# Optimization experiments

Hardware: AMD Instinct MI355X
Metric: run time of the kernel (lower is better)

The kernel has to match this reference:

```python
import jax, jax.numpy as jnp
import numpy as np

B, L, H, DK, DV, D, FC, NL = 8, 2016, 4, 32, 32, 256, 64, 3
EPS = 1e-5
SCALE = 1.0 / np.sqrt(float(D))  # module uses 1/sqrt(d_model), not 1/sqrt(dim_k)


def _ln(x, g, b):
    m = jnp.mean(x, axis=-1, keepdims=True)
    v = jnp.mean((x - m) ** 2, axis=-1, keepdims=True)
    return (x - m) * jax.lax.rsqrt(v + EPS) * g + b


def setup_inputs() -> dict:
    key = jax.random.key(0)
    ks = iter(jax.random.split(key, 32))

    def lin(k, shape, fan_in):
        # torch nn.Linear default: U(-1/sqrt(fan_in), 1/sqrt(fan_in))
        lim = 1.0 / np.sqrt(float(fan_in))
        return jax.random.uniform(k, shape, minval=-lim, maxval=lim, dtype=jnp.float32)

    inp = {
        'x': jax.random.normal(next(ks), (B, L, 2), dtype=jnp.float32),
        'in_w': lin(next(ks), (2, D), 2),
        'in_b': lin(next(ks), (D,), 2),
        'qw': lin(next(ks), (NL, D, H * DK), D),
        'qb': lin(next(ks), (NL, H * DK), D),
        'kw': lin(next(ks), (NL, D, H * DK), D),
        'kb': lin(next(ks), (NL, H * DK), D),
        'vw': lin(next(ks), (NL, D, H * DV), D),
        'vb': lin(next(ks), (NL, H * DV), D),
        'ow': lin(next(ks), (NL, H * DV, D), H * DV),
        'ob': lin(next(ks), (NL, D), H * DV),
        'f1w': lin(next(ks), (NL, D, FC), D),
        'f1b': lin(next(ks), (NL, FC), D),
        'f2w': lin(next(ks), (NL, FC, D), FC),
        'f2b': lin(next(ks), (NL, D), FC),
        'n1g': jnp.ones((NL, D), jnp.float32),
        'n1b': jnp.zeros((NL, D), jnp.float32),
        'n2g': jnp.ones((NL, D), jnp.float32),
        'n2b': jnp.zeros((NL, D), jnp.float32),
        'o1w': lin(next(ks), (D, D), D),
        'o1b': lin(next(ks), (D,), D),
        'o2w': lin(next(ks), (D, 2), D),
        'o2b': lin(next(ks), (2,), D),
    }
    return inp


def reference(x, in_w, in_b, qw, qb, kw, kb, vw, vb, ow, ob,
              f1w, f1b, f2w, f2b, n1g, n1b, n2g, n2b,
              o1w, o1b, o2w, o2b):
    h = x @ in_w + in_b  # (B, L, D)
    attns = []
    for i in range(NL):
        Q = (h @ qw[i] + qb[i]).reshape(B, L, H, DK)
        K = (h @ kw[i] + kb[i]).reshape(B, L, H, DK)
        V = (h @ vw[i] + vb[i]).reshape(B, L, H, DV)
        scores = jnp.einsum('blhe,bshe->bhls', Q, K) * SCALE  # (B,H,L,L)
        scores = jax.nn.softmax(scores, axis=-1)
        o = jnp.einsum('bhls,bshd->blhd', scores, V).reshape(B, L, H * DV)
        h = _ln(h + (o @ ow[i] + ob[i]), n1g[i], n1b[i])  # dropout is identity at eval
        ff = jax.nn.relu(h @ f1w[i] + f1b[i]) @ f2w[i] + f2b[i]
        h = _ln(h + ff, n2g[i], n2b[i])
        attns.append(scores)
    out = jax.nn.relu(h @ o1w + o1b) @ o2w + o2b  # (B, L, 2)
    return (out, jnp.stack(attns))
```

## Files before the change

### kernel.cpp

```cpp
#include <hip/hip_runtime.h>

typedef __attribute__((ext_vector_type(8))) short bh8;
typedef __attribute__((ext_vector_type(4))) float f32x4;

#define NB   8
#define NLAY 3
#define LSEQ 2016
#define NH   4
#define DM   256
#define FCN  64
#define MR   (NB*LSEQ)
#define SCL  0.0625f
#define SP   2024

__device__ __forceinline__ float b2f(unsigned short u) {
  union { unsigned int i; float f; } c; c.i = ((unsigned int)u) << 16; return c.f;
}
__device__ __forceinline__ unsigned short f2b(float f) {
  union { float f; unsigned int i; } c; c.f = f;
  unsigned int r = c.i + 0x7fffu + ((c.i >> 16) & 1u);
  return (unsigned short)(r >> 16);
}

__global__ __launch_bounds__(256) void k_f2bf(const float* __restrict__ s,
    unsigned short* __restrict__ d, int n) {
  int i = blockIdx.x * 256 + threadIdx.x;
  if (i < n) d[i] = f2b(s[i]);
}

__global__ __launch_bounds__(256) void k_embed(const float* __restrict__ x,
    const float* __restrict__ w, const float* __restrict__ bias,
    float* __restrict__ h, unsigned short* __restrict__ hb) {
  int m = blockIdx.x, d = threadIdx.x;
  float v = x[m*2] * w[d] + x[m*2+1] * w[DM + d] + bias[d];
  size_t idx = (size_t)m * DM + d;
  h[idx] = v;
  hb[idx] = f2b(v);
}

template<int MODE, int RELU>
__global__ __launch_bounds__(256) void k_gemm(
    const unsigned short* __restrict__ A, const unsigned short* __restrict__ W,
    const float* __restrict__ bias, const float* __restrict__ res,
    void* __restrict__ outp, int M, int N, int K)
{
  __shared__ unsigned short As[64 * 40];
  __shared__ unsigned short Ws[64 * 40];
  const int t = threadIdx.x;
  const int lane = t & 63, w = t >> 6;
  const int bm = blockIdx.y << 6, bn = blockIdx.x << 6;
  const int mw = (w & 1) << 5, nw = (w >> 1) << 5;
  const int q = lane >> 4, r = lane & 15;
  const int am = t >> 2, akc = (t & 3) << 3;
  const int wk = t >> 3, wnc = (t & 7) << 3;

  f32x4 zero = {0.f, 0.f, 0.f, 0.f};
  f32x4 acc[2][2] = {{zero, zero}, {zero, zero}};

  for (int k0 = 0; k0 < K; k0 += 32) {
    uint4 av = *(const uint4*)(A + (size_t)(bm + am) * K + k0 + akc);
    *(uint4*)(As + am * 40 + akc) = av;
    union { uint4 u; unsigned short s[8]; } wv;
    wv.u = *(const uint4*)(W + (size_t)(k0 + wk) * N + bn + wnc);
    #pragma unroll
    for (int j = 0; j < 8; ++j) Ws[(wnc + j) * 40 + wk] = wv.s[j];
    __syncthreads();

    bh8 a0 = *(const bh8*)(As + (mw + r) * 40 + (q << 3));
    bh8 a1 = *(const bh8*)(As + (mw + 16 + r) * 40 + (q << 3));
    bh8 b0 = *(const bh8*)(Ws + (nw + r) * 40 + (q << 3));
    bh8 b1 = *(const bh8*)(Ws + (nw + 16 + r) * 40 + (q << 3));
    acc[0][0] = __builtin_amdgcn_mfma_f32_16x16x32_bf16(a0, b0, acc[0][0], 0, 0, 0);
    acc[0][1] = __builtin_amdgcn_mfma_f32_16x16x32_bf16(a0, b1, acc[0][1], 0, 0, 0);
    acc[1][0] = __builtin_amdgcn_mfma_f32_16x16x32_bf16(a1, b0, acc[1][0], 0, 0, 0);
    acc[1][1] = __builtin_amdgcn_mfma_f32_16x16x32_bf16(a1, b1, acc[1][1], 0, 0, 0);
    __syncthreads();
  }

  #pragma unroll
  for (int mi = 0; mi < 2; ++mi)
  #pragma unroll
  for (int ni = 0; ni < 2; ++ni)
  #pragma unroll
  for (int rr = 0; rr < 4; ++rr) {
    int gm = bm + mw + (mi << 4) + (q << 2) + rr;
    int gn = bn + nw + (ni << 4) + r;
    float v = acc[mi][ni][rr] + bias[gn];
    if (RELU) v = v > 0.f ? v : 0.f;
    if (MODE == 0) {
      ((unsigned short*)outp)[(size_t)gm * N + gn] = f2b(v);
    } else if (MODE == 1) {
      int b = gm / LSEQ, l = gm - b * LSEQ;
      int hh = gn >> 5, e = gn & 31;
      ((unsigned short*)outp)[((((size_t)b * NH + hh) * LSEQ + l) << 5) + e] = f2b(v);
    } else if (MODE == 2) {
      int b = gm / LSEQ, l = gm - b * LSEQ;
      int hh = gn >> 5, e = gn & 31;
      ((unsigned short*)outp)[(((size_t)b * NH + hh) * 32 + e) * LSEQ + l] = f2b(v);
    } else {
      size_t idx = (size_t)gm * DM + gn;
      ((float*)outp)[idx] = v + res[idx];
    }
  }
}

__global__ __launch_bounds__(256) void k_ln(const float* __restrict__ y,
    const float* __restrict__ g, const float* __restrict__ bta,
    float* __restrict__ h, unsigned short* __restrict__ hb)
{
  int t = threadIdx.x, lane = t & 63, w = t >> 6;
  int row = blockIdx.x * 4 + w;
  const float* yr = y + (size_t)row * DM;
  float4 v = *(const float4*)(yr + lane * 4);
  float s = v.x + v.y + v.z + v.w;
  float sq = v.x * v.x + v.y * v.y + v.z * v.z + v.w * v.w;
  #pragma unroll
  for (int m = 1; m < 64; m <<= 1) { s += __shfl_xor(s, m, 64); sq += __shfl_xor(sq, m, 64); }
  float mean = s * (1.f / 256.f);
  float var = sq * (1.f / 256.f) - mean * mean;
  float rs = rsqrtf(var + 1e-5f);
  float4 gg = *(const float4*)(g + lane * 4);
  float4 bb = *(const float4*)(bta + lane * 4);
  float4 o;
  o.x = (v.x - mean) * rs * gg.x + bb.x;
  o.y = (v.y - mean) * rs * gg.y + bb.y;
  o.z = (v.z - mean) * rs * gg.z + bb.z;
  o.w = (v.w - mean) * rs * gg.w + bb.w;
  *(float4*)(h + (size_t)row * DM + lane * 4) = o;
  ushort4 u;
  u.x = f2b(o.x); u.y = f2b(o.y); u.z = f2b(o.z); u.w = f2b(o.w);
  *(ushort4*)(hb + (size_t)row * DM + lane * 4) = u;
}

__global__ __launch_bounds__(256) void k_attn(
    const unsigned short* __restrict__ Qb, const unsigned short* __restrict__ Kb,
    const unsigned short* __restrict__ Vt, float* __restrict__ Pout,
    unsigned short* __restrict__ ao)
{
  __shared__ unsigned short S[16 * SP];
  __shared__ float red[4 * 16 * 32];
  __shared__ float rinv[16];
  const int t = threadIdx.x, lane = t & 63, w = t >> 6;
  const int bid = blockIdx.x;
  const int rb = bid % 126, bh = bid / 126;
  const int l0 = rb << 4;
  const int q = lane >> 4, r = lane & 15;

  bh8 qf = *(const bh8*)(Qb + (((size_t)bh * LSEQ + l0 + r) << 5) + (q << 3));
  for (int st = w; st < 126; st += 4) {
    int s0 = st << 4;
    bh8 kf = *(const bh8*)(Kb + (((size_t)bh * LSEQ + s0 + r) << 5) + (q << 3));
    f32x4 c = {0.f, 0.f, 0.f, 0.f};
    c = __builtin_amdgcn_mfma_f32_16x16x32_bf16(qf, kf, c, 0, 0, 0);
    #pragma unroll
    for (int rr = 0; rr < 4; ++rr)
      S[(q * 4 + rr) * SP + s0 + r] = f2b(c[rr] * SCL);
  }
  __syncthreads();

  {
    int row = t >> 4, c = t & 15;
    float mx = -1e30f;
    for (int col = c; col < LSEQ; col += 16)
      mx = fmaxf(mx, b2f(S[row * SP + col]));
    #pragma unroll
    for (int m = 1; m < 16; m <<= 1) mx = fmaxf(mx, __shfl_xor(mx, m, 64));
    float sum = 0.f;
    for (int col = c; col < LSEQ; col += 16) {
      float e = __expf(b2f(S[row * SP + col]) - mx);
      sum += e;
      S[row * SP + col] = f2b(e);
    }
    #pragma unroll
    for (int m = 1; m < 16; m <<= 1) sum += __shfl_xor(sum, m, 64);
    if (c == 0) rinv[row] = 1.f / sum;
  }
  __syncthreads();

  float* prow0 = Pout + (size_t)bh * LSEQ * LSEQ + (size_t)l0 * LSEQ;
  for (int row = 0; row < 16; ++row) {
    float iv = rinv[row];
    float* pr = prow0 + (size_t)row * LSEQ;
    for (int col = t; col < LSEQ; col += 256)
      pr[col] = b2f(S[row * SP + col]) * iv;
  }

  f32x4 o0 = {0.f, 0.f, 0.f, 0.f}, o1 = {0.f, 0.f, 0.f, 0.f};
  const unsigned short* vtb = Vt + (size_t)bh * 32 * LSEQ;
  for (int st = w; st < 63; st += 4) {
    int s0 = st << 5;
    bh8 pf = *(const bh8*)(S + r * SP + s0 + (q << 3));
    bh8 v0 = *(const bh8*)(vtb + (size_t)r * LSEQ + s0 + (q << 3));
    bh8 v1 = *(const bh8*)(vtb + (size_t)(16 + r) * LSEQ + s0 + (q << 3));
    o0 = __builtin_amdgcn_mfma_f32_16x16x32_bf16(pf, v0, o0, 0, 0, 0);
    o1 = __builtin_amdgcn_mfma_f32_16x16x32_bf16(pf, v1, o1, 0, 0, 0);
  }
  float* rw = red + w * 512;
  #pragma unroll
  for (int rr = 0; rr < 4; ++rr) {
    rw[(q * 4 + rr) * 32 + r] = o0[rr];
    rw[(q * 4 + rr) * 32 + 16 + r] = o1[rr];
  }
  __syncthreads();
  for (int idx = t; idx < 512; idx += 256) {
    int row = idx >> 5, d = idx & 31;
    float v = red[idx] + red[512 + idx] + red[1024 + idx] + red[1536 + idx];
    v *= rinv[row];
    int b = bh >> 2, hh = bh & 3;
    ao[(size_t)(b * LSEQ + l0 + row) * 128 + (hh << 5) + d] = f2b(v);
  }
}

__global__ __launch_bounds__(256) void k_head(const unsigned short* __restrict__ t1,
    const float* __restrict__ o2w, const float* __restrict__ o2b,
    float* __restrict__ outp)
{
  int t = threadIdx.x, lane = t & 63, w = t >> 6;
  int row = blockIdx.x * 4 + w;
  union { ushort4 u; unsigned short s[4]; } pk;
  pk.u = *(const ushort4*)(t1 + (size_t)row * DM + lane * 4);
  float a0 = 0.f, a1 = 0.f;
  #pragma unroll
  for (int j = 0; j < 4; ++j) {
    float xv = b2f(pk.s[j]);
    int k = lane * 4 + j;
    a0 += xv * o2w[k * 2];
    a1 += xv * o2w[k * 2 + 1];
  }
  #pragma unroll
  for (int m = 1; m < 64; m <<= 1) { a0 += __shfl_xor(a0, m, 64); a1 += __shfl_xor(a1, m, 64); }
  if (lane == 0) {
    outp[(size_t)row * 2]     = a0 + o2b[0];
    outp[(size_t)row * 2 + 1] = a1 + o2b[1];
  }
}

extern "C" void kernel_launch(void* const* d_in, const int* in_sizes, int n_in,
                              void* d_out, int out_size, void* d_ws, size_t ws_size,
                              hipStream_t stream) {
  const float* x    = (const float*)d_in[0];
  const float* in_w = (const float*)d_in[1];
  const float* in_b = (const float*)d_in[2];
  const float* qw   = (const float*)d_in[3];
  const float* qb   = (const float*)d_in[4];
  const float* kw   = (const float*)d_in[5];
  const float* kb   = (const float*)d_in[6];
  const float* vw   = (const float*)d_in[7];
  const float* vb   = (const float*)d_in[8];
  const float* ow   = (const float*)d_in[9];
  const float* ob   = (const float*)d_in[10];
  const float* f1w  = (const float*)d_in[11];
  const float* f1b  = (const float*)d_in[12];
  const float* f2w  = (const float*)d_in[13];
  const float* f2b  = (const float*)d_in[14];
  const float* n1g  = (const float*)d_in[15];
  const float* n1b  = (const float*)d_in[16];
  const float* n2g  = (const float*)d_in[17];
  const float* n2b  = (const float*)d_in[18];
  const float* o1w  = (const float*)d_in[19];
  const float* o1b  = (const float*)d_in[20];
  const float* o2w  = (const float*)d_in[21];
  const float* o2b  = (const float*)d_in[22];

  char* p = (char*)d_ws;
  auto alloc = [&](size_t bytes) { char* r = p; p += (bytes + 255) & ~(size_t)255; return r; };
  float*          h    = (float*)alloc((size_t)MR * DM * 4);
  unsigned short* hb   = (unsigned short*)alloc((size_t)MR * DM * 2);
  float*          tmp  = (float*)alloc((size_t)MR * DM * 4);
  unsigned short* Qb   = (unsigned short*)alloc((size_t)MR * 128 * 2);
  unsigned short* Kb   = (unsigned short*)alloc((size_t)MR * 128 * 2);
  unsigned short* Vt   = (unsigned short*)alloc((size_t)MR * 128 * 2);
  unsigned short* ao   = (unsigned short*)alloc((size_t)MR * 128 * 2);
  unsigned short* Fb   = (unsigned short*)alloc((size_t)MR * FCN * 2);
  unsigned short* t1   = (unsigned short*)alloc((size_t)MR * DM * 2);
  unsigned short* qwb  = (unsigned short*)alloc(98304 * 2);
  unsigned short* kwb  = (unsigned short*)alloc(98304 * 2);
  unsigned short* vwb  = (unsigned short*)alloc(98304 * 2);
  unsigned short* owb  = (unsigned short*)alloc(98304 * 2);
  unsigned short* f1wb = (unsigned short*)alloc(49152 * 2);
  unsigned short* f2wb = (unsigned short*)alloc(49152 * 2);
  unsigned short* o1wb = (unsigned short*)alloc(65536 * 2);

  k_f2bf<<<(98304 + 255) / 256, 256, 0, stream>>>(qw, qwb, 98304);
  k_f2bf<<<(98304 + 255) / 256, 256, 0, stream>>>(kw, kwb, 98304);
  k_f2bf<<<(98304 + 255) / 256, 256, 0, stream>>>(vw, vwb, 98304);
  k_f2bf<<<(98304 + 255) / 256, 256, 0, stream>>>(ow, owb, 98304);
  k_f2bf<<<(49152 + 255) / 256, 256, 0, stream>>>(f1w, f1wb, 49152);
  k_f2bf<<<(49152 + 255) / 256, 256, 0, stream>>>(f2w, f2wb, 49152);
  k_f2bf<<<(65536 + 255) / 256, 256, 0, stream>>>(o1w, o1wb, 65536);

  k_embed<<<MR, 256, 0, stream>>>(x, in_w, in_b, h, hb);

  float* outp = (float*)d_out;
  for (int i = 0; i < NLAY; ++i) {
    k_gemm<1, 0><<<dim3(2, 252), 256, 0, stream>>>(hb, qwb + i * 32768, qb + i * 128, nullptr, Qb, MR, 128, 256);
    k_gemm<1, 0><<<dim3(2, 252), 256, 0, stream>>>(hb, kwb + i * 32768, kb + i * 128, nullptr, Kb, MR, 128, 256);
    k_gemm<2, 0><<<dim3(2, 252), 256, 0, stream>>>(hb, vwb + i * 32768, vb + i * 128, nullptr, Vt, MR, 128, 256);
    k_attn<<<4032, 256, 0, stream>>>(Qb, Kb, Vt,
        outp + 32256 + (size_t)i * NB * NH * LSEQ * LSEQ, ao);
    k_gemm<3, 0><<<dim3(4, 252), 256, 0, stream>>>(ao, owb + i * 32768, ob + i * 256, h, tmp, MR, 256, 128);
    k_ln<<<MR / 4, 256, 0, stream>>>(tmp, n1g + i * 256, n1b + i * 256, h, hb);
    k_gemm<0, 1><<<dim3(1, 252), 256, 0, stream>>>(hb, f1wb + i * 16384, f1b + i * 64, nullptr, Fb, MR, 64, 256);
    k_gemm<3, 0><<<dim3(4, 252), 256, 0, stream>>>(Fb, f2wb + i * 16384, f2b + i * 256, h, tmp, MR, 256, 64);
    k_ln<<<MR / 4, 256, 0, stream>>>(tmp, n2g + i * 256, n2b + i * 256, h, hb);
  }
  k_gemm<0, 1><<<dim3(4, 252), 256, 0, stream>>>(hb, o1wb, o1b, nullptr, t1, MR, 256, 256);
  k_head<<<MR / 4, 256, 0, stream>>>(t1, o2w, o2b, outp);
}
```

Measured before the change: 2.572 ms.

## Rewrite attention as two-pass online softmax with per-wave tiles and prefetch GEMM loads

```diff
diff --git a/kernel.cpp b/kernel.cpp
--- a/kernel.cpp
+++ b/kernel.cpp
@@ -11,7 +11,7 @@
 #define FCN  64
 #define MR   (NB*LSEQ)
 #define SCL  0.0625f
-#define SP   2024
+#define TP   40
 
 __device__ __forceinline__ float b2f(unsigned short u) {
   union { unsigned int i; float f; } c; c.i = ((unsigned int)u) << 16; return c.f;
@@ -20,6 +20,11 @@
   union { float f; unsigned int i; } c; c.f = f;
   unsigned int r = c.i + 0x7fffu + ((c.i >> 16) & 1u);
   return (unsigned short)(r >> 16);
+}
+__device__ __forceinline__ unsigned int pk_bf16(float lo, float hi) {
+  unsigned int r;
+  asm("v_cvt_pk_bf16_f32 %0, %1, %2" : "=v"(r) : "v"(lo), "v"(hi));
+  return r;
 }
 
 __global__ __launch_bounds__(256) void k_f2bf(const float* __restrict__ s,
@@ -42,7 +47,7 @@
 __global__ __launch_bounds__(256) void k_gemm(
     const unsigned short* __restrict__ A, const unsigned short* __restrict__ W,
     const float* __restrict__ bias, const float* __restrict__ res,
-    void* __restrict__ outp, int M, int N, int K)
+    void* __restrict__ outp, float oscale, int M, int N, int K)
 {
   __shared__ unsigned short As[64 * 40];
   __shared__ unsigned short Ws[64 * 40];
@@ -57,14 +62,20 @@
   f32x4 zero = {0.f, 0.f, 0.f, 0.f};
   f32x4 acc[2][2] = {{zero, zero}, {zero, zero}};
 
+  uint4 av = *(const uint4*)(A + (size_t)(bm + am) * K + akc);
+  union { uint4 u; unsigned short s[8]; } wv;
+  wv.u = *(const uint4*)(W + (size_t)wk * N + bn + wnc);
+
   for (int k0 = 0; k0 < K; k0 += 32) {
-    uint4 av = *(const uint4*)(A + (size_t)(bm + am) * K + k0 + akc);
     *(uint4*)(As + am * 40 + akc) = av;
-    union { uint4 u; unsigned short s[8]; } wv;
-    wv.u = *(const uint4*)(W + (size_t)(k0 + wk) * N + bn + wnc);
     #pragma unroll
     for (int j = 0; j < 8; ++j) Ws[(wnc + j) * 40 + wk] = wv.s[j];
     __syncthreads();
+
+    if (k0 + 32 < K) {
+      av = *(const uint4*)(A + (size_t)(bm + am) * K + k0 + 32 + akc);
+      wv.u = *(const uint4*)(W + (size_t)(k0 + 32 + wk) * N + bn + wnc);
+    }
 
     bh8 a0 = *(const bh8*)(As + (mw + r) * 40 + (q << 3));
     bh8 a1 = *(const bh8*)(As + (mw + 16 + r) * 40 + (q << 3));
@@ -85,7 +96,7 @@
   for (int rr = 0; rr < 4; ++rr) {
     int gm = bm + mw + (mi << 4) + (q << 2) + rr;
     int gn = bn + nw + (ni << 4) + r;
-    float v = acc[mi][ni][rr] + bias[gn];
+    float v = (acc[mi][ni][rr] + bias[gn]) * oscale;
     if (RELU) v = v > 0.f ? v : 0.f;
     if (MODE == 0) {
       ((unsigned short*)outp)[(size_t)gm * N + gn] = f2b(v);
@@ -137,9 +148,10 @@
     const unsigned short* __restrict__ Vt, float* __restrict__ Pout,
     unsigned short* __restrict__ ao)
 {
-  __shared__ unsigned short S[16 * SP];
-  __shared__ float red[4 * 16 * 32];
-  __shared__ float rinv[16];
+  __shared__ __align__(16) unsigned short tile[4][2][16 * TP];
+  __shared__ float mbuf[4][16][2];
+  __shared__ float rowstat[16][2];
+  __shared__ float red[4 * 512];
   const int t = threadIdx.x, lane = t & 63, w = t >> 6;
   const int bid = blockIdx.x;
   const int rb = bid % 126, bh = bid / 126;
@@ -147,54 +159,91 @@
   const int q = lane >> 4, r = lane & 15;
 
   bh8 qf = *(const bh8*)(Qb + (((size_t)bh * LSEQ + l0 + r) << 5) + (q << 3));
-  for (int st = w; st < 126; st += 4) {
-    int s0 = st << 4;
-    bh8 kf = *(const bh8*)(Kb + (((size_t)bh * LSEQ + s0 + r) << 5) + (q << 3));
-    f32x4 c = {0.f, 0.f, 0.f, 0.f};
-    c = __builtin_amdgcn_mfma_f32_16x16x32_bf16(qf, kf, c, 0, 0, 0);
+  const unsigned short* kb = Kb + (((size_t)bh * LSEQ) << 5) + (q << 3);
+
+  const int stb = w << 5;
+  const int ste = (w == 3) ? 126 : stb + 32;
+
+  float m = -1e30f, l = 0.f;
+  for (int st = stb; st < ste; st += 2) {
+    int kbase = st << 4;
+    bh8 kf0 = *(const bh8*)(kb + ((size_t)(kbase + r) << 5));
+    bh8 kf1 = *(const bh8*)(kb + ((size_t)(kbase + 16 + r) << 5));
+    f32x4 z = {0.f, 0.f, 0.f, 0.f};
+    f32x4 c0 = __builtin_amdgcn_mfma_f32_16x16x32_bf16(kf0, qf, z, 0, 0, 0);
+    f32x4 c1 = __builtin_amdgcn_mfma_f32_16x16x32_bf16(kf1, qf, z, 0, 0, 0);
+    float mx = fmaxf(fmaxf(fmaxf(c0[0], c0[1]), fmaxf(c0[2], c0[3])),
+                     fmaxf(fmaxf(c1[0], c1[1]), fmaxf(c1[2], c1[3])));
+    float mn = fmaxf(m, mx);
+    float sc = __expf(m - mn);
+    float s = ((__expf(c0[0]-mn) + __expf(c0[1]-mn)) + (__expf(c0[2]-mn) + __expf(c0[3]-mn)))
+            + ((__expf(c1[0]-mn) + __expf(c1[1]-mn)) + (__expf(c1[2]-mn) + __expf(c1[3]-mn)));
+    l = l * sc + s;
+    m = mn;
+  }
+  #pragma unroll
+  for (int mk = 16; mk < 64; mk <<= 1) {
+    float mo = __shfl_xor(m, mk, 64);
+    float lo = __shfl_xor(l, mk, 64);
+    float mn = fmaxf(m, mo);
+    l = l * __expf(m - mn) + lo * __expf(mo - mn);
+    m = mn;
+  }
+  if (q == 0) { mbuf[w][r][0] = m; mbuf[w][r][1] = l; }
+  __syncthreads();
+  if (t < 16) {
+    float mm = -1e30f, ll = 0.f;
     #pragma unroll
-    for (int rr = 0; rr < 4; ++rr)
-      S[(q * 4 + rr) * SP + s0 + r] = f2b(c[rr] * SCL);
+    for (int wv = 0; wv < 4; ++wv) {
+      float m2 = mbuf[wv][t][0], l2 = mbuf[wv][t][1];
+      float mn = fmaxf(mm, m2);
+      ll = ll * __expf(mm - mn) + l2 * __expf(m2 - mn);
+      mm = mn;
+    }
+    rowstat[t][0] = mm;
+    rowstat[t][1] = 1.f / ll;
   }
   __syncthreads();
-
-  {
-    int row = t >> 4, c = t & 15;
-    float mx = -1e30f;
-    for (int col = c; col < LSEQ; col += 16)
-      mx = fmaxf(mx, b2f(S[row * SP + col]));
-    #pragma unroll
-    for (int m = 1; m < 16; m <<= 1) mx = fmaxf(mx, __shfl_xor(mx, m, 64));
-    float sum = 0.f;
-    for (int col = c; col < LSEQ; col += 16) {
-      float e = __expf(b2f(S[row * SP + col]) - mx);
-      sum += e;
-      S[row * SP + col] = f2b(e);
-    }
-    #pragma unroll
-    for (int m = 1; m < 16; m <<= 1) sum += __shfl_xor(sum, m, 64);
-    if (c == 0) rinv[row] = 1.f / sum;
-  }
-  __syncthreads();
-
-  float* prow0 = Pout + (size_t)bh * LSEQ * LSEQ + (size_t)l0 * LSEQ;
-  for (int row = 0; row < 16; ++row) {
-    float iv = rinv[row];
-    float* pr = prow0 + (size_t)row * LSEQ;
-    for (int col = t; col < LSEQ; col += 256)
-      pr[col] = b2f(S[row * SP + col]) * iv;
-  }
+  const float mrow = rowstat[r][0];
+  const float rinv = rowstat[r][1];
 
   f32x4 o0 = {0.f, 0.f, 0.f, 0.f}, o1 = {0.f, 0.f, 0.f, 0.f};
   const unsigned short* vtb = Vt + (size_t)bh * 32 * LSEQ;
-  for (int st = w; st < 63; st += 4) {
-    int s0 = st << 5;
-    bh8 pf = *(const bh8*)(S + r * SP + s0 + (q << 3));
-    bh8 v0 = *(const bh8*)(vtb + (size_t)r * LSEQ + s0 + (q << 3));
-    bh8 v1 = *(const bh8*)(vtb + (size_t)(16 + r) * LSEQ + s0 + (q << 3));
-    o0 = __builtin_amdgcn_mfma_f32_16x16x32_bf16(pf, v0, o0, 0, 0, 0);
-    o1 = __builtin_amdgcn_mfma_f32_16x16x32_bf16(pf, v1, o1, 0, 0, 0);
-  }
+  float* prow = Pout + (size_t)bh * LSEQ * LSEQ + (size_t)(l0 + r) * LSEQ + (q << 2);
+  unsigned short* tA = &tile[w][0][0];
+  unsigned short* tB = &tile[w][1][0];
+  int pb = 0;
+  for (int st = stb; st < ste; st += 2, pb ^= 1) {
+    int kbase = st << 4;
+    bh8 kf0 = *(const bh8*)(kb + ((size_t)(kbase + r) << 5));
+    bh8 kf1 = *(const bh8*)(kb + ((size_t)(kbase + 16 + r) << 5));
+    f32x4 z = {0.f, 0.f, 0.f, 0.f};
+    f32x4 c0 = __builtin_amdgcn_mfma_f32_16x16x32_bf16(kf0, qf, z, 0, 0, 0);
+    f32x4 c1 = __builtin_amdgcn_mfma_f32_16x16x32_bf16(kf1, qf, z, 0, 0, 0);
+    float e0 = __expf(c0[0]-mrow), e1 = __expf(c0[1]-mrow);
+    float e2 = __expf(c0[2]-mrow), e3 = __expf(c0[3]-mrow);
+    float e4 = __expf(c1[0]-mrow), e5 = __expf(c1[1]-mrow);
+    float e6 = __expf(c1[2]-mrow), e7 = __expf(c1[3]-mrow);
+    float4 p0, p1;
+    p0.x = e0*rinv; p0.y = e1*rinv; p0.z = e2*rinv; p0.w = e3*rinv;
+    p1.x = e4*rinv; p1.y = e5*rinv; p1.z = e6*rinv; p1.w = e7*rinv;
+    *(float4*)(prow + kbase) = p0;
+    *(float4*)(prow + kbase + 16) = p1;
+    unsigned short* tp = pb ? tB : tA;
+    uint2 u0, u1;
+    u0.x = pk_bf16(e0, e1); u0.y = pk_bf16(e2, e3);
+    u1.x = pk_bf16(e4, e5); u1.y = pk_bf16(e6, e7);
+    __builtin_amdgcn_wave_barrier();
+    *(uint2*)(tp + r * TP + (q << 2)) = u0;
+    *(uint2*)(tp + r * TP + 16 + (q << 2)) = u1;
+    __builtin_amdgcn_wave_barrier();
+    bh8 pf = *(const bh8*)(tp + r * TP + (q << 3));
+    bh8 va = *(const bh8*)(vtb + (size_t)r * LSEQ + kbase + (q << 3));
+    bh8 vb = *(const bh8*)(vtb + (size_t)(16 + r) * LSEQ + kbase + (q << 3));
+    o0 = __builtin_amdgcn_mfma_f32_16x16x32_bf16(pf, va, o0, 0, 0, 0);
+    o1 = __builtin_amdgcn_mfma_f32_16x16x32_bf16(pf, vb, o1, 0, 0, 0);
+  }
+
   float* rw = red + w * 512;
   #pragma unroll
   for (int rr = 0; rr < 4; ++rr) {
@@ -205,7 +254,7 @@
   for (int idx = t; idx < 512; idx += 256) {
     int row = idx >> 5, d = idx & 31;
     float v = red[idx] + red[512 + idx] + red[1024 + idx] + red[1536 + idx];
-    v *= rinv[row];
+    v *= rowstat[row][1];
     int b = bh >> 2, hh = bh & 3;
     ao[(size_t)(b * LSEQ + l0 + row) * 128 + (hh << 5) + d] = f2b(v);
   }
@@ -293,17 +342,17 @@
 
   float* outp = (float*)d_out;
   for (int i = 0; i < NLAY; ++i) {
-    k_gemm<1, 0><<<dim3(2, 252), 256, 0, stream>>>(hb, qwb + i * 32768, qb + i * 128, nullptr, Qb, MR, 128, 256);
-    k_gemm<1, 0><<<dim3(2, 252), 256, 0, stream>>>(hb, kwb + i * 32768, kb + i * 128, nullptr, Kb, MR, 128, 256);
-    k_gemm<2, 0><<<dim3(2, 252), 256, 0, stream>>>(hb, vwb + i * 32768, vb + i * 128, nullptr, Vt, MR, 128, 256);
+    k_gemm<1, 0><<<dim3(2, 252), 256, 0, stream>>>(hb, qwb + i * 32768, qb + i * 128, nullptr, Qb, SCL, MR, 128, 256);
+    k_gemm<1, 0><<<dim3(2, 252), 256, 0, stream>>>(hb, kwb + i * 32768, kb + i * 128, nullptr, Kb, 1.f, MR, 128, 256);
+    k_gemm<2, 0><<<dim3(2, 252), 256, 0, stream>>>(hb, vwb + i * 32768, vb + i * 128, nullptr, Vt, 1.f, MR, 128, 256);
     k_attn<<<4032, 256, 0, stream>>>(Qb, Kb, Vt,
         outp + 32256 + (size_t)i * NB * NH * LSEQ * LSEQ, ao);
-    k_gemm<3, 0><<<dim3(4, 252), 256, 0, stream>>>(ao, owb + i * 32768, ob + i * 256, h, tmp, MR, 256, 128);
+    k_gemm<3, 0><<<dim3(4, 252), 256, 0, stream>>>(ao, owb + i * 32768, ob + i * 256, h, tmp, 1.f, MR, 256, 128);
     k_ln<<<MR / 4, 256, 0, stream>>>(tmp, n1g + i * 256, n1b + i * 256, h, hb);
-    k_gemm<0, 1><<<dim3(1, 252), 256, 0, stream>>>(hb, f1wb + i * 16384, f1b + i * 64, nullptr, Fb, MR, 64, 256);
-    k_gemm<3, 0><<<dim3(4, 252), 256, 0, stream>>>(Fb, f2wb + i * 16384, f2b + i * 256, h, tmp, MR, 256, 64);
+    k_gemm<0, 1><<<dim3(1, 252), 256, 0, stream>>>(hb, f1wb + i * 16384, f1b + i * 64, nullptr, Fb, 1.f, MR, 64, 256);
+    k_gemm<3, 0><<<dim3(4, 252), 256, 0, stream>>>(Fb, f2wb + i * 16384, f2b + i * 256, h, tmp, 1.f, MR, 256, 64);
     k_ln<<<MR / 4, 256, 0, stream>>>(tmp, n2g + i * 256, n2b + i * 256, h, hb);
   }
-  k_gemm<0, 1><<<dim3(4, 252), 256, 0, stream>>>(hb, o1wb, o1b, nullptr, t1, MR, 256, 256);
+  k_gemm<0, 1><<<dim3(4, 252), 256, 0, stream>>>(hb, o1wb, o1b, nullptr, t1, 1.f, MR, 256, 256);
   k_head<<<MR / 4, 256, 0, stream>>>(t1, o2w, o2b, outp);
 }
```

New measurement: 2.129 ms. 1.21x faster.
